# Performance work log

Hardware: AMD Instinct MI355X
Metric: run time of the kernel (lower is better)

## Reference

```python
import jax, jax.numpy as jnp
import numpy as np

H_DIM = 1024
GATE_DIM = 128


def setup_inputs() -> dict:
    key = jax.random.key(0)
    ks = jax.random.split(key, 7)
    B, L = 32, 2048
    bound_g = 1.0 / np.sqrt(GATE_DIM)
    bound_l = 1.0 / np.sqrt(GATE_DIM)
    return {
        "x": jax.random.normal(ks[0], (B, L, H_DIM), dtype=jnp.float32),
        # GRUCell params (PyTorch layout: rows ordered [r; z; n])
        "weight_ih": jax.random.uniform(ks[1], (3 * GATE_DIM, H_DIM), minval=-bound_g, maxval=bound_g, dtype=jnp.float32),
        "weight_hh": jax.random.uniform(ks[2], (3 * GATE_DIM, GATE_DIM), minval=-bound_g, maxval=bound_g, dtype=jnp.float32),
        "bias_ih": jax.random.uniform(ks[3], (3 * GATE_DIM,), minval=-bound_g, maxval=bound_g, dtype=jnp.float32),
        "bias_hh": jax.random.uniform(ks[4], (3 * GATE_DIM,), minval=-bound_g, maxval=bound_g, dtype=jnp.float32),
        # output linear (gate_dim -> 1)
        "lin_w": jax.random.uniform(ks[5], (1, GATE_DIM), minval=-bound_l, maxval=bound_l, dtype=jnp.float32),
        "lin_b": jax.random.uniform(ks[6], (1,), minval=-bound_l, maxval=bound_l, dtype=jnp.float32),
    }


def reference(x, weight_ih, weight_hh, bias_ih, bias_hh, lin_w, lin_b):
    """Faithful to the original PingHead.forward: `s` is never updated, so every
    timestep runs the GRUCell against a ZERO hidden state. weight_hh @ h == 0,
    leaving only bias_hh contributions. This lets us vectorize over (B, L)."""
    G = GATE_DIM
    # input projection for all gates: (B, L, 3G)
    gi = jnp.einsum('blh,gh->blg', x, weight_ih) + bias_ih
    i_r, i_z, i_n = gi[..., :G], gi[..., G:2 * G], gi[..., 2 * G:]
    b_hr, b_hz, b_hn = bias_hh[:G], bias_hh[G:2 * G], bias_hh[2 * G:]
    r = jax.nn.sigmoid(i_r + b_hr)
    z = jax.nn.sigmoid(i_z + b_hz)
    n = jnp.tanh(i_n + r * b_hn)
    h = (1.0 - z) * n  # + z * 0 (hidden state is always zero)
    # linear(gate_dim -> 1), squeeze last dim -> (B, L)
    out = jnp.einsum('blg,og->blo', h, lin_w) + lin_b
    return out[..., 0]
```

## Files before the change

kernel.cpp:

```cpp
#include <hip/hip_runtime.h>

#define H_DIM   1024
#define G_DIM   128
#define N_DIM   384
#define M_TOTAL 65536
#define BM      64

typedef _Float16 half8  __attribute__((ext_vector_type(8)));
typedef _Float16 half4  __attribute__((ext_vector_type(4)));
typedef __fp16   fp16x2 __attribute__((ext_vector_type(2)));
typedef float    f32x4  __attribute__((ext_vector_type(4)));

__device__ __forceinline__ float fast_sigmoid(float v) {
    return 1.0f / (1.0f + __expf(-v));
}
__device__ __forceinline__ float fast_tanh(float v) {
    return 1.0f - 2.0f / (__expf(2.0f * v) + 1.0f);
}

__device__ __forceinline__ half4 cvt4(f32x4 v) {
    fp16x2 p0 = __builtin_amdgcn_cvt_pkrtz(v[0], v[1]);
    fp16x2 p1 = __builtin_amdgcn_cvt_pkrtz(v[2], v[3]);
    half4 h;
    h[0] = (_Float16)p0[0]; h[1] = (_Float16)p0[1];
    h[2] = (_Float16)p1[0]; h[3] = (_Float16)p1[1];
    return h;
}

__global__ __launch_bounds__(256) void prep_w_kernel(const float* __restrict__ w,
                                                     _Float16* __restrict__ wf) {
    int gid  = blockIdx.x * 256 + threadIdx.x;
    int lane = gid & 63;
    int fid  = gid >> 6;
    int ktg  = fid & 31;
    int ct   = fid >> 5;
    int col  = ct * 16 + (lane & 15);
    int kb   = ktg * 32 + (lane >> 4) * 8;
    const f32x4* src = (const f32x4*)(w + (size_t)col * H_DIM + kb);
    f32x4 v0 = src[0], v1 = src[1];
    half8 h;
    #pragma unroll
    for (int j = 0; j < 4; ++j) { h[j] = (_Float16)v0[j]; h[4 + j] = (_Float16)v1[j]; }
    *(half8*)(wf + (size_t)gid * 8) = h;
}

#define FENCE() asm volatile("" ::: "memory")
#define WAITLGKM0() { FENCE(); __builtin_amdgcn_s_waitcnt(0xC07F); FENCE(); }
#define BARRW()     { WAITLGKM0(); __builtin_amdgcn_s_barrier(); FENCE(); }

__global__ __launch_bounds__(512, 4) void ping_main_kernel(
    const float* __restrict__ x, const _Float16* __restrict__ wf,
    const float* __restrict__ bias_ih, const float* __restrict__ bias_hh,
    const float* __restrict__ lin_w, const float* __restrict__ lin_b,
    float* __restrict__ out)
{
    __shared__ _Float16 shX[4 * 2048];
    __shared__ float sh_out[BM];

    const int t    = threadIdx.x;
    const int lane = t & 63;
    const int wv   = t >> 6;
    const int ln   = lane & 15;
    const int quad = lane >> 4;

    if (t < BM) sh_out[t] = 0.0f;

    const size_t row0 = (size_t)blockIdx.x * BM;

    const int drow = wv * 8 + (lane >> 3);
    const int dcol = (lane & 7) * 4;
    const float* xsrc = x + (row0 + drow) * (size_t)H_DIM + dcol;
    _Float16* wdst = &shX[drow * 32 + dcol];

    const char* aBase = (const char*)&shX[0] + ln * 64 + quad * 16;

    const _Float16* pb[3];
    #pragma unroll
    for (int i = 0; i < 3; ++i)
        pb[i] = wf + (size_t)((wv + 8 * i) * 32) * 512 + lane * 8;

    f32x4 acc[3][4];
    #pragma unroll
    for (int i = 0; i < 3; ++i)
        #pragma unroll
        for (int rt = 0; rt < 4; ++rt)
            acc[i][rt] = (f32x4){0.f, 0.f, 0.f, 0.f};

    f32x4 g[4];
    half8 bf[2][3];

    g[0] = *(const f32x4*)(xsrc);
    g[1] = *(const f32x4*)(xsrc + 32);
    g[2] = *(const f32x4*)(xsrc + 64);
    g[3] = *(const f32x4*)(xsrc + 96);
    #pragma unroll
    for (int i = 0; i < 3; ++i) {
        bf[0][i] = *(const half8*)(pb[i]);
        bf[1][i] = *(const half8*)(pb[i] + 512);
    }
    *(half4*)(wdst)        = cvt4(g[0]);
    *(half4*)(wdst + 2048) = cvt4(g[1]);
    g[0] = *(const f32x4*)(xsrc + 128);
    BARRW();

#define STEP(K, DO_G, DO_B, DO_S, DO_BAR) { \
    _Pragma("unroll") \
    for (int rt = 0; rt < 4; ++rt) { \
        half8 afr = *(const half8*)(aBase + ((K) & 3) * 4096 + rt * 1024); \
        _Pragma("unroll") \
        for (int i = 0; i < 3; ++i) \
            acc[i][rt] = __builtin_amdgcn_mfma_f32_16x16x32_f16(afr, bf[(K) & 1][i], acc[i][rt], 0, 0, 0); \
    } \
    if (DO_G) g[((K) + 1) & 3] = *(const f32x4*)(xsrc + (size_t)((K) + 5) * 32); \
    if (DO_B) { \
        _Pragma("unroll") \
        for (int i = 0; i < 3; ++i) \
            bf[(K) & 1][i] = *(const half8*)(pb[i] + (size_t)((K) + 2) * 512); \
    } \
    if (DO_S) *(half4*)(wdst + (((K) + 2) & 3) * 2048) = cvt4(g[((K) + 2) & 3]); \
    if (DO_BAR) BARRW(); }

    for (int kb = 0; kb < 24; kb += 4) {
        STEP(kb + 0, true, true, true, false);
        STEP(kb + 1, true, true, true, true);
        STEP(kb + 2, true, true, true, false);
        STEP(kb + 3, true, true, true, true);
    }
    STEP(24, true,  true,  true,  false);
    STEP(25, true,  true,  true,  true);
    STEP(26, true,  true,  true,  false);
    STEP(27, false, true,  true,  true);
    STEP(28, false, true,  true,  false);
    STEP(29, false, true,  true,  true);
    STEP(30, false, false, false, false);
    STEP(31, false, false, false, false);

    const int g_col = 16 * wv + ln;
    const float b_ir = bias_ih[g_col];
    const float b_iz = bias_ih[G_DIM + g_col];
    const float b_in = bias_ih[2 * G_DIM + g_col];
    const float b_hr = bias_hh[g_col];
    const float b_hz = bias_hh[G_DIM + g_col];
    const float b_hn = bias_hh[2 * G_DIM + g_col];
    const float lw   = lin_w[g_col];

    #pragma unroll
    for (int rt = 0; rt < 4; ++rt) {
        #pragma unroll
        for (int reg = 0; reg < 4; ++reg) {
            const float r = fast_sigmoid(acc[0][rt][reg] + b_ir + b_hr);
            const float z = fast_sigmoid(acc[1][rt][reg] + b_iz + b_hz);
            const float n = fast_tanh(acc[2][rt][reg] + b_in + r * b_hn);
            float v = lw * (1.0f - z) * n;
            v += __shfl_xor(v, 1);
            v += __shfl_xor(v, 2);
            v += __shfl_xor(v, 4);
            v += __shfl_xor(v, 8);
            if (ln == 0) atomicAdd(&sh_out[rt * 16 + quad * 4 + reg], v);
        }
    }

    __syncthreads();
    if (t < BM) out[row0 + t] = sh_out[t] + lin_b[0];
}

extern "C" void kernel_launch(void* const* d_in, const int* in_sizes, int n_in,
                              void* d_out, int out_size, void* d_ws, size_t ws_size,
                              hipStream_t stream) {
    const float* x      = (const float*)d_in[0];
    const float* w_ih   = (const float*)d_in[1];
    const float* b_ih   = (const float*)d_in[3];
    const float* b_hh   = (const float*)d_in[4];
    const float* lin_w  = (const float*)d_in[5];
    const float* lin_b  = (const float*)d_in[6];
    float* out          = (float*)d_out;
    _Float16* wf        = (_Float16*)d_ws;

    hipLaunchKernelGGL(prep_w_kernel, dim3((N_DIM / 16) * 32 * 64 / 256), dim3(256), 0, stream,
                       w_ih, wf);
    hipLaunchKernelGGL(ping_main_kernel, dim3(M_TOTAL / BM), dim3(512), 0, stream,
                       x, wf, b_ih, b_hh, lin_w, lin_b, out);
}
```

Before: 392.1 us.

## Interleave per-wave weight fragments and deepen B/X register prefetch

Reorganizes the fp16 weight workspace so each wave's three gate fragments for a k-step are contiguous (24 halves per lane), and loads two k-steps of B fragments at once every other step. The X global prefetch distance is increased by one step. This aims to reduce the number of global load instructions and hide more latency, at the cost of more registers for the doubled bf buffer, which could hurt occupancy.

After: 393.1 us. Within noise of the previous version (+0.2%).

```diff
diff --git a/kernel.cpp b/kernel.cpp
--- a/kernel.cpp
+++ b/kernel.cpp
@@ -29,19 +29,24 @@
 
 __global__ __launch_bounds__(256) void prep_w_kernel(const float* __restrict__ w,
                                                      _Float16* __restrict__ wf) {
-    int gid  = blockIdx.x * 256 + threadIdx.x;
-    int lane = gid & 63;
-    int fid  = gid >> 6;
-    int ktg  = fid & 31;
-    int ct   = fid >> 5;
-    int col  = ct * 16 + (lane & 15);
+    int tid  = blockIdx.x * 256 + threadIdx.x;
+    int lane = tid & 63;
+    int grp  = tid >> 6;
+    int wv   = grp >> 5;
+    int ktg  = grp & 31;
+    int ln   = lane & 15;
     int kb   = ktg * 32 + (lane >> 4) * 8;
-    const f32x4* src = (const f32x4*)(w + (size_t)col * H_DIM + kb);
-    f32x4 v0 = src[0], v1 = src[1];
-    half8 h;
+    _Float16* dst = wf + ((size_t)grp * 64 + lane) * 24;
     #pragma unroll
-    for (int j = 0; j < 4; ++j) { h[j] = (_Float16)v0[j]; h[4 + j] = (_Float16)v1[j]; }
-    *(half8*)(wf + (size_t)gid * 8) = h;
+    for (int i = 0; i < 3; ++i) {
+        int col = (wv + 8 * i) * 16 + ln;
+        const f32x4* src = (const f32x4*)(w + (size_t)col * H_DIM + kb);
+        f32x4 v0 = src[0], v1 = src[1];
+        half8 h;
+        #pragma unroll
+        for (int j = 0; j < 4; ++j) { h[j] = (_Float16)v0[j]; h[4 + j] = (_Float16)v1[j]; }
+        *(half8*)(dst + i * 8) = h;
+    }
 }
 
 #define FENCE() asm volatile("" ::: "memory")
@@ -74,10 +79,7 @@
 
     const char* aBase = (const char*)&shX[0] + ln * 64 + quad * 16;
 
-    const _Float16* pb[3];
-    #pragma unroll
-    for (int i = 0; i < 3; ++i)
-        pb[i] = wf + (size_t)((wv + 8 * i) * 32) * 512 + lane * 8;
+    const _Float16* pb = wf + ((size_t)(wv * 32) * 64 + lane) * 24;
 
     f32x4 acc[3][4];
     #pragma unroll
@@ -87,20 +89,26 @@
             acc[i][rt] = (f32x4){0.f, 0.f, 0.f, 0.f};
 
     f32x4 g[4];
-    half8 bf[2][3];
+    half8 bf[2][6];
+
+#define BLOAD(S) { \
+    const _Float16* pbS = pb + (size_t)(S) * 1536; \
+    _Pragma("unroll") \
+    for (int i = 0; i < 3; ++i) { \
+        bf[((S) >> 1) & 1][i]     = *(const half8*)(pbS + i * 8); \
+        bf[((S) >> 1) & 1][3 + i] = *(const half8*)(pbS + 1536 + i * 8); \
+    } }
 
     g[0] = *(const f32x4*)(xsrc);
     g[1] = *(const f32x4*)(xsrc + 32);
+    BLOAD(0);
+    BLOAD(2);
     g[2] = *(const f32x4*)(xsrc + 64);
     g[3] = *(const f32x4*)(xsrc + 96);
-    #pragma unroll
-    for (int i = 0; i < 3; ++i) {
-        bf[0][i] = *(const half8*)(pb[i]);
-        bf[1][i] = *(const half8*)(pb[i] + 512);
-    }
     *(half4*)(wdst)        = cvt4(g[0]);
     *(half4*)(wdst + 2048) = cvt4(g[1]);
     g[0] = *(const f32x4*)(xsrc + 128);
+    g[1] = *(const f32x4*)(xsrc + 160);
     BARRW();
 
 #define STEP(K, DO_G, DO_B, DO_S, DO_BAR) { \
@@ -109,29 +117,25 @@
         half8 afr = *(const half8*)(aBase + ((K) & 3) * 4096 + rt * 1024); \
         _Pragma("unroll") \
         for (int i = 0; i < 3; ++i) \
-            acc[i][rt] = __builtin_amdgcn_mfma_f32_16x16x32_f16(afr, bf[(K) & 1][i], acc[i][rt], 0, 0, 0); \
-    } \
-    if (DO_G) g[((K) + 1) & 3] = *(const f32x4*)(xsrc + (size_t)((K) + 5) * 32); \
-    if (DO_B) { \
-        _Pragma("unroll") \
-        for (int i = 0; i < 3; ++i) \
-            bf[(K) & 1][i] = *(const half8*)(pb[i] + (size_t)((K) + 2) * 512); \
+            acc[i][rt] = __builtin_amdgcn_mfma_f32_16x16x32_f16(afr, bf[((K) >> 1) & 1][((K) & 1) * 3 + i], acc[i][rt], 0, 0, 0); \
     } \
     if (DO_S) *(half4*)(wdst + (((K) + 2) & 3) * 2048) = cvt4(g[((K) + 2) & 3]); \
+    if (DO_B) BLOAD((K) + 3); \
+    if (DO_G) g[((K) + 6) & 3] = *(const f32x4*)(xsrc + (size_t)((K) + 6) * 32); \
     if (DO_BAR) BARRW(); }
 
     for (int kb = 0; kb < 24; kb += 4) {
-        STEP(kb + 0, true, true, true, false);
-        STEP(kb + 1, true, true, true, true);
-        STEP(kb + 2, true, true, true, false);
-        STEP(kb + 3, true, true, true, true);
+        STEP(kb + 0, true, false, true, false);
+        STEP(kb + 1, true, true,  true, true);
+        STEP(kb + 2, true, false, true, false);
+        STEP(kb + 3, true, true,  true, true);
     }
-    STEP(24, true,  true,  true,  false);
+    STEP(24, true,  false, true,  false);
     STEP(25, true,  true,  true,  true);
-    STEP(26, true,  true,  true,  false);
+    STEP(26, false, false, true,  false);
     STEP(27, false, true,  true,  true);
-    STEP(28, false, true,  true,  false);
-    STEP(29, false, true,  true,  true);
+    STEP(28, false, false, true,  false);
+    STEP(29, false, false, true,  true);
     STEP(30, false, false, false, false);
     STEP(31, false, false, false, false);
 
@@ -176,7 +180,7 @@
     float* out          = (float*)d_out;
     _Float16* wf        = (_Float16*)d_ws;
 
-    hipLaunchKernelGGL(prep_w_kernel, dim3((N_DIM / 16) * 32 * 64 / 256), dim3(256), 0, stream,
+    hipLaunchKernelGGL(prep_w_kernel, dim3(64), dim3(256), 0, stream,
                        w_ih, wf);
     hipLaunchKernelGGL(ping_main_kernel, dim3(M_TOTAL / BM), dim3(512), 0, stream,
                        x, wf, b_ih, b_hh, lin_w, lin_b, out);
```
